# Performance work log

Hardware: AMD Instinct MI355X
Metric: run time of the kernel (lower is better)

## Reference

```python
import jax, jax.numpy as jnp
import numpy as np

NUM_HEADS = 16
LN_EPS = 1e-5


def _layer_norm(x, g, b):
    m = x.mean(-1, keepdims=True)
    v = x.var(-1, keepdims=True)
    return (x - m) / jnp.sqrt(v + LN_EPS) * g + b


def setup_inputs() -> dict:
    key = jax.random.key(0)
    ks = jax.random.split(key, 4)
    Bq, Bk, Nk, C = 128, 128, 256, 1024
    return {
        "qx": jax.random.normal(ks[0], (Bq, 1, C), jnp.float32),
        "kx": jax.random.normal(ks[1], (Bk, Nk, C), jnp.float32),
        "gq": jnp.ones((C,), jnp.float32),
        "bq": jnp.zeros((C,), jnp.float32),
        "gk": jnp.ones((C,), jnp.float32),
        "bk": jnp.zeros((C,), jnp.float32),
        "Wq": jax.random.normal(ks[2], (C, C), jnp.float32) * (C ** -0.5),
        "Wk": jax.random.normal(ks[3], (C, C), jnp.float32) * (C ** -0.5),
    }


def reference(qx, kx, gq, bq, gk, bk, Wq, Wk):
    H = NUM_HEADS
    Bq, _, C = qx.shape  # qx: [Bq, 1, C]
    Bk, Nk, _ = kx.shape  # kx: [Bk, Nk, C]
    hd = C // H
    scale = hd ** -0.5
    # LayerNorm + linear projections (nn.Linear: x @ W.T, no bias)
    q = (_layer_norm(qx, gq, bq) @ Wq.T).reshape(Bq, H, hd)       # [Bq, H, hd] (Nq=1 squeezed)
    k = (_layer_norm(kx, gk, bk) @ Wk.T).reshape(Bk, Nk, H, hd)   # [Bk, Nk, H, hd]
    # Full bipartite cross-batch attention scores: [Bq, Bk, H, Nk]
    attn = jnp.einsum('qhc,knhc->qkhn', q, k) * scale
    attn = jax.nn.softmax(attn, axis=-1)
    # v = kx broadcast over heads in original einsum 'khnc,qkhn->qkc';
    # equivalent: sum attn over heads, then contract over Nk.
    w = attn.sum(axis=2)                                           # [Bq, Bk, Nk]
    x = jnp.einsum('knc,qkn->qkc', kx, w)                          # [Bq, Bk, C]
    return x
```

## Files before the change

### kernel.cpp

```cpp
#include <hip/hip_runtime.h>


typedef unsigned short ushort_t;
typedef __bf16 bf16x8 __attribute__((ext_vector_type(8)));
typedef float f32x4 __attribute__((ext_vector_type(4)));

#define AS1 __attribute__((address_space(1)))
#define AS3 __attribute__((address_space(3)))

__device__ __forceinline__ void gload_lds16(const void* g, void* l) {
  __builtin_amdgcn_global_load_lds((const AS1 unsigned int*)g, (AS3 unsigned int*)l, 16, 0, 0);
}

__device__ __forceinline__ ushort_t f2bf(float f) {
  unsigned u = __float_as_uint(f);
  unsigned r = u + 0x7FFFu + ((u >> 16) & 1u);
  return (ushort_t)(r >> 16);
}

__global__ __launch_bounds__(256) void cvt_bf16_kernel(const float* __restrict__ src,
                                                       ushort_t* __restrict__ dst, int n4) {
  int i = blockIdx.x * 256 + threadIdx.x;
  if (i < n4) {
    float4 v = ((const float4*)src)[i];
    ushort4 o;
    o.x = f2bf(v.x); o.y = f2bf(v.y); o.z = f2bf(v.z); o.w = f2bf(v.w);
    ((ushort4*)dst)[i] = o;
  }
}

__global__ __launch_bounds__(256) void ln_kernel(const float* __restrict__ kx,
                                                 const float* __restrict__ qx,
                                                 const float* __restrict__ gk,
                                                 const float* __restrict__ bk,
                                                 const float* __restrict__ gq,
                                                 const float* __restrict__ bq,
                                                 ushort_t* __restrict__ kln,
                                                 ushort_t* __restrict__ qln) {
  int row = blockIdx.x;
  const float* src; ushort_t* dst; const float* g; const float* bb;
  if (row < 32768) {
    src = kx + (size_t)row * 1024; dst = kln + (size_t)row * 1024; g = gk; bb = bk;
  } else {
    int r = row - 32768;
    src = qx + (size_t)r * 1024; dst = qln + (size_t)r * 1024; g = gq; bb = bq;
  }
  int tid = threadIdx.x;
  float4 v = ((const float4*)src)[tid];
  float s  = v.x + v.y + v.z + v.w;
  float s2 = v.x*v.x + v.y*v.y + v.z*v.z + v.w*v.w;
  #pragma unroll
  for (int off = 1; off < 64; off <<= 1) {
    s  += __shfl_xor(s, off);
    s2 += __shfl_xor(s2, off);
  }
  __shared__ float red[8];
  int wid = tid >> 6, lane = tid & 63;
  if (lane == 0) { red[wid] = s; red[4 + wid] = s2; }
  __syncthreads();
  s  = red[0] + red[1] + red[2] + red[3];
  s2 = red[4] + red[5] + red[6] + red[7];
  float mean = s * (1.0f / 1024.0f);
  float var  = s2 * (1.0f / 1024.0f) - mean * mean;
  float rstd = rsqrtf(var + 1e-5f);
  float4 gg = ((const float4*)g)[tid];
  float4 b4 = ((const float4*)bb)[tid];
  ushort4 o;
  o.x = f2bf((v.x - mean) * rstd * gg.x + b4.x);
  o.y = f2bf((v.y - mean) * rstd * gg.y + b4.y);
  o.z = f2bf((v.z - mean) * rstd * gg.z + b4.z);
  o.w = f2bf((v.w - mean) * rstd * gg.w + b4.w);
  ((ushort4*)dst)[tid] = o;
}

#define BM 128
#define BN 128
#define BK 32

__global__ __launch_bounds__(256) void gemm_bt_kernel(const ushort_t* __restrict__ A,
                                                      const ushort_t* __restrict__ Bt,
                                                      ushort_t* __restrict__ C,
                                                      int M, int N, int K) {
  __shared__ ushort_t As[2][BM * BK];
  __shared__ ushort_t Bs[2][BN * BK];
  const int tid  = threadIdx.x;
  const int lane = tid & 63;
  const int wid  = tid >> 6;

  const int Mt = M >> 7, Nt = N >> 7;
  const int nwg = Mt * Nt;
  const int qq = nwg >> 3, r8 = nwg & 7;
  const int xcd = blockIdx.x & 7, idx = blockIdx.x >> 3;
  const int wg = (xcd < r8 ? xcd * (qq + 1) : r8 * (qq + 1) + (xcd - r8) * qq) + idx;
  const int mt = wg / Nt, nt = wg - mt * Nt;
  const size_t m0 = (size_t)mt * BM, n0 = (size_t)nt * BN;

  const int NTILE = K / BK;
  const int rlo = lane >> 2;
  const int cl  = lane & 3;

  f32x4 acc[4][4];
  #pragma unroll
  for (int i = 0; i < 4; ++i)
    #pragma unroll
    for (int j = 0; j < 4; ++j) acc[i][j] = (f32x4){0.f, 0.f, 0.f, 0.f};

  #pragma unroll
  for (int c = 0; c < 2; ++c) {
    int row = (wid << 5) + (c << 4) + rlo;
    int gch = cl ^ (row & 3);
    gload_lds16(A  + (m0 + row) * (size_t)K + gch * 8, &As[0][((wid << 5) + (c << 4)) * BK]);
    gload_lds16(Bt + (n0 + row) * (size_t)K + gch * 8, &Bs[0][((wid << 5) + (c << 4)) * BK]);
  }

  const int g = lane >> 4, rr = lane & 15;
  const int wr = wid >> 1, wc = wid & 1;

  for (int t = 0; t < NTILE; ++t) {
    __syncthreads();
    if (t + 1 < NTILE) {
      int k0 = (t + 1) * BK;
      #pragma unroll
      for (int c = 0; c < 2; ++c) {
        int row = (wid << 5) + (c << 4) + rlo;
        int gch = cl ^ (row & 3);
        gload_lds16(A  + (m0 + row) * (size_t)K + k0 + gch * 8,
                    &As[(t + 1) & 1][((wid << 5) + (c << 4)) * BK]);
        gload_lds16(Bt + (n0 + row) * (size_t)K + k0 + gch * 8,
                    &Bs[(t + 1) & 1][((wid << 5) + (c << 4)) * BK]);
      }
    }
    const ushort_t* as = As[t & 1];
    const ushort_t* bs = Bs[t & 1];
    bf16x8 af[4], bfr[4];
    #pragma unroll
    for (int i = 0; i < 4; ++i) {
      int rowA = (wr << 6) + (i << 4) + rr;
      int chA  = g ^ (rowA & 3);
      af[i] = *(const bf16x8*)&as[rowA * BK + chA * 8];
      int rowB = (wc << 6) + (i << 4) + rr;
      int chB  = g ^ (rowB & 3);
      bfr[i] = *(const bf16x8*)&bs[rowB * BK + chB * 8];
    }
    #pragma unroll
    for (int i = 0; i < 4; ++i)
      #pragma unroll
      for (int j = 0; j < 4; ++j)
        acc[i][j] = __builtin_amdgcn_mfma_f32_16x16x32_bf16(af[i], bfr[j], acc[i][j], 0, 0, 0);
  }

  #pragma unroll
  for (int i = 0; i < 4; ++i)
    #pragma unroll
    for (int j = 0; j < 4; ++j)
      #pragma unroll
      for (int rg = 0; rg < 4; ++rg) {
        size_t row = m0 + (wr << 6) + (i << 4) + (g << 2) + rg;
        size_t col = n0 + (wc << 6) + (j << 4) + rr;
        C[row * (size_t)N + col] = f2bf(acc[i][j][rg]);
      }
}

__global__ __launch_bounds__(256, 2) void attn_kernel(const ushort_t* __restrict__ qp,
                                                      const ushort_t* __restrict__ kk,
                                                      const float* __restrict__ kx,
                                                      float* __restrict__ xout) {
  __shared__ float pbuf[32][260];
  __shared__ ushort_t wlds[32 * 256];

  const int tid = threadIdx.x, lane = tid & 63, wid = tid >> 6;
  const int g = lane >> 4, rr = lane & 15;

  const int b = blockIdx.x;
  const int wg = (b & 7) * 64 + (b >> 3);
  const int kb = wg >> 2;
  const int q0 = (wg & 3) * 32;

  const int qg = wid & 1, hs = wid >> 1;
  const int q16 = q0 + (qg << 4);

  float w_acc[16][4];
  #pragma unroll
  for (int t = 0; t < 16; ++t)
    #pragma unroll
    for (int r = 0; r < 4; ++r) w_acc[t][r] = 0.f;

  const ushort_t* qrow = qp + (size_t)(q16 + rr) * 1024;
  const ushort_t* krow = kk + ((size_t)kb * 256 + rr) * 1024;

  for (int hp = 0; hp < 8; ++hp) {
    const int h = hp * 2 + hs;
    const int co = h * 64 + g * 8;
    bf16x8 aq0 = *(const bf16x8*)(qrow + co);
    bf16x8 aq1 = *(const bf16x8*)(qrow + co + 32);
    f32x4 s[16];
    #pragma unroll
    for (int t = 0; t < 16; ++t) {
      const ushort_t* kr = krow + (size_t)(t * 16) * 1024 + co;
      bf16x8 b0 = *(const bf16x8*)(kr);
      bf16x8 b1 = *(const bf16x8*)(kr + 32);
      f32x4 a = (f32x4){0.f, 0.f, 0.f, 0.f};
      a = __builtin_amdgcn_mfma_f32_16x16x32_bf16(aq0, b0, a, 0, 0, 0);
      a = __builtin_amdgcn_mfma_f32_16x16x32_bf16(aq1, b1, a, 0, 0, 0);
      s[t] = a;
    }
    #pragma unroll
    for (int r = 0; r < 4; ++r) {
      float mx = s[0][r];
      #pragma unroll
      for (int t = 1; t < 16; ++t) mx = fmaxf(mx, s[t][r]);
      mx = fmaxf(mx, __shfl_xor(mx, 1));
      mx = fmaxf(mx, __shfl_xor(mx, 2));
      mx = fmaxf(mx, __shfl_xor(mx, 4));
      mx = fmaxf(mx, __shfl_xor(mx, 8));
      float sum = 0.f;
      float e[16];
      #pragma unroll
      for (int t = 0; t < 16; ++t) {
        e[t] = __expf((s[t][r] - mx) * 0.125f);
        sum += e[t];
      }
      sum += __shfl_xor(sum, 1);
      sum += __shfl_xor(sum, 2);
      sum += __shfl_xor(sum, 4);
      sum += __shfl_xor(sum, 8);
      float inv = 1.0f / sum;
      #pragma unroll
      for (int t = 0; t < 16; ++t) w_acc[t][r] += e[t] * inv;
    }
  }

  __syncthreads();
  if (hs == 1) {
    #pragma unroll
    for (int t = 0; t < 16; ++t)
      #pragma unroll
      for (int r = 0; r < 4; ++r)
        pbuf[(qg << 4) + (g << 2) + r][t * 16 + rr] = w_acc[t][r];
  }
  __syncthreads();
  if (hs == 0) {
    #pragma unroll
    for (int t = 0; t < 16; ++t)
      #pragma unroll
      for (int r = 0; r < 4; ++r) {
        int q = (qg << 4) + (g << 2) + r;
        int n = t * 16 + rr;
        float v = w_acc[t][r] + pbuf[q][n];
        wlds[q * 256 + (((n >> 3) ^ (q & 7)) << 3) + (n & 7)] = f2bf(v);
      }
  }
  __syncthreads();

  const int cw = wid << 8;
  f32x4 acc2[2][16];
  #pragma unroll
  for (int m2 = 0; m2 < 2; ++m2)
    #pragma unroll
    for (int t2 = 0; t2 < 16; ++t2) acc2[m2][t2] = (f32x4){0.f, 0.f, 0.f, 0.f};

  for (int nc = 0; nc < 8; ++nc) {
    const int n0 = nc * 32;
    bf16x8 pa[2];
    #pragma unroll
    for (int m2 = 0; m2 < 2; ++m2) {
      int q = (m2 << 4) + rr;
      pa[m2] = *(const bf16x8*)&wlds[q * 256 + ((((nc << 2) + g) ^ (q & 7)) << 3)];
    }
    const float* kxb = kx + ((size_t)kb * 256 + n0 + g * 8) * 1024;
    #pragma unroll
    for (int t2 = 0; t2 < 16; ++t2) {
      const int c = cw + t2 * 16 + rr;
      float f[8];
      #pragma unroll
      for (int j = 0; j < 8; ++j) f[j] = kxb[(size_t)j * 1024 + c];
      bf16x8 bb;
      #pragma unroll
      for (int j = 0; j < 8; ++j) bb[j] = (__bf16)f[j];
      acc2[0][t2] = __builtin_amdgcn_mfma_f32_16x16x32_bf16(pa[0], bb, acc2[0][t2], 0, 0, 0);
      acc2[1][t2] = __builtin_amdgcn_mfma_f32_16x16x32_bf16(pa[1], bb, acc2[1][t2], 0, 0, 0);
    }
  }

  #pragma unroll
  for (int m2 = 0; m2 < 2; ++m2)
    #pragma unroll
    for (int t2 = 0; t2 < 16; ++t2)
      #pragma unroll
      for (int rg = 0; rg < 4; ++rg) {
        int q = q0 + (m2 << 4) + (g << 2) + rg;
        int c = cw + t2 * 16 + rr;
        xout[((size_t)q * 128 + kb) * 1024 + c] = acc2[m2][t2][rg];
      }
}

extern "C" void kernel_launch(void* const* d_in, const int* in_sizes, int n_in,
                              void* d_out, int out_size, void* d_ws, size_t ws_size,
                              hipStream_t stream) {
  const float* qx = (const float*)d_in[0];
  const float* kx = (const float*)d_in[1];
  const float* gq = (const float*)d_in[2];
  const float* bq = (const float*)d_in[3];
  const float* gk = (const float*)d_in[4];
  const float* bk = (const float*)d_in[5];
  const float* Wq = (const float*)d_in[6];
  const float* Wk = (const float*)d_in[7];

  char* ws = (char*)d_ws;
  ushort_t* kkp   = (ushort_t*)(ws);
  ushort_t* qln   = (ushort_t*)(ws + 67108864);
  ushort_t* qproj = (ushort_t*)(ws + 67371008);
  ushort_t* Wqb   = (ushort_t*)(ws + 67633152);
  ushort_t* Wkb   = (ushort_t*)(ws + 69730304);
  ushort_t* kln  = (ushort_t*)d_out;
  float*    xout = (float*)d_out;

  cvt_bf16_kernel<<<1024, 256, 0, stream>>>(Wq, Wqb, 262144);
  cvt_bf16_kernel<<<1024, 256, 0, stream>>>(Wk, Wkb, 262144);
  ln_kernel<<<32896, 256, 0, stream>>>(kx, qx, gk, bk, gq, bq, kln, qln);
  gemm_bt_kernel<<<8, 256, 0, stream>>>(qln, Wqb, qproj, 128, 1024, 1024);
  gemm_bt_kernel<<<2048, 256, 0, stream>>>(kln, Wkb, kkp, 32768, 1024, 1024);
  attn_kernel<<<512, 256, 0, stream>>>(qproj, kkp, kx, xout);
}
```

Measured before the change: 283.1 us.

## Split fused attention into separate scores and PV kernels with larger tiles

The fused attention kernel becomes two kernels. A scores kernel uses 512 threads, splits the 16 heads across four waves, reduces their partial softmax weights through LDS in two stages, and writes the bf16 head-summed weights to a workspace buffer. A separate PV kernel then computes the 128x128 output tiles per key batch as a GEMM. In that GEMM each block covers all 128 queries, so every kx element is read and converted once per block instead of four times. The cost is one extra launch and a global round trip for the weight matrix, and the workspace layout is rearranged so wbuf reuses the qln region.

```diff
diff --git a/kernel.cpp b/kernel.cpp
--- a/kernel.cpp
+++ b/kernel.cpp
@@ -161,12 +161,10 @@
       }
 }
 
-__global__ __launch_bounds__(256, 2) void attn_kernel(const ushort_t* __restrict__ qp,
-                                                      const ushort_t* __restrict__ kk,
-                                                      const float* __restrict__ kx,
-                                                      float* __restrict__ xout) {
-  __shared__ float pbuf[32][260];
-  __shared__ ushort_t wlds[32 * 256];
+__global__ __launch_bounds__(512, 4) void scores_kernel(const ushort_t* __restrict__ qp,
+                                                        const ushort_t* __restrict__ kk,
+                                                        ushort_t* __restrict__ wbuf) {
+  __shared__ float pbuf[2][2][16][258];
 
   const int tid = threadIdx.x, lane = tid & 63, wid = tid >> 6;
   const int g = lane >> 4, rr = lane & 15;
@@ -176,7 +174,7 @@
   const int kb = wg >> 2;
   const int q0 = (wg & 3) * 32;
 
-  const int qg = wid & 1, hs = wid >> 1;
+  const int qg = wid >> 2, hs = wid & 3;
   const int q16 = q0 + (qg << 4);
 
   float w_acc[16][4];
@@ -188,8 +186,8 @@
   const ushort_t* qrow = qp + (size_t)(q16 + rr) * 1024;
   const ushort_t* krow = kk + ((size_t)kb * 256 + rr) * 1024;
 
-  for (int hp = 0; hp < 8; ++hp) {
-    const int h = hp * 2 + hs;
+  for (int hp = 0; hp < 4; ++hp) {
+    const int h = hp * 4 + hs;
     const int co = h * 64 + g * 8;
     bf16x8 aq0 = *(const bf16x8*)(qrow + co);
     bf16x8 aq1 = *(const bf16x8*)(qrow + co + 32);
@@ -231,66 +229,96 @@
   }
 
   __syncthreads();
-  if (hs == 1) {
+  if (hs >= 2) {
     #pragma unroll
     for (int t = 0; t < 16; ++t)
       #pragma unroll
       for (int r = 0; r < 4; ++r)
-        pbuf[(qg << 4) + (g << 2) + r][t * 16 + rr] = w_acc[t][r];
+        pbuf[qg][hs - 2][(g << 2) + r][t * 16 + rr] = w_acc[t][r];
+  }
+  __syncthreads();
+  if (hs < 2) {
+    #pragma unroll
+    for (int t = 0; t < 16; ++t)
+      #pragma unroll
+      for (int r = 0; r < 4; ++r)
+        w_acc[t][r] += pbuf[qg][hs][(g << 2) + r][t * 16 + rr];
+    if (hs == 1) {
+      #pragma unroll
+      for (int t = 0; t < 16; ++t)
+        #pragma unroll
+        for (int r = 0; r < 4; ++r)
+          pbuf[qg][1][(g << 2) + r][t * 16 + rr] = w_acc[t][r];
+    }
   }
   __syncthreads();
   if (hs == 0) {
+    ushort_t* wb = wbuf + (size_t)kb * 32768;
     #pragma unroll
     for (int t = 0; t < 16; ++t)
       #pragma unroll
       for (int r = 0; r < 4; ++r) {
-        int q = (qg << 4) + (g << 2) + r;
-        int n = t * 16 + rr;
-        float v = w_acc[t][r] + pbuf[q][n];
-        wlds[q * 256 + (((n >> 3) ^ (q & 7)) << 3) + (n & 7)] = f2bf(v);
-      }
-  }
-  __syncthreads();
-
-  const int cw = wid << 8;
-  f32x4 acc2[2][16];
-  #pragma unroll
-  for (int m2 = 0; m2 < 2; ++m2)
-    #pragma unroll
-    for (int t2 = 0; t2 < 16; ++t2) acc2[m2][t2] = (f32x4){0.f, 0.f, 0.f, 0.f};
+        float v = w_acc[t][r] + pbuf[qg][1][(g << 2) + r][t * 16 + rr];
+        wb[(size_t)(q16 + (g << 2) + r) * 256 + t * 16 + rr] = f2bf(v);
+      }
+  }
+}
+
+__global__ __launch_bounds__(256, 4) void pv_kernel(const ushort_t* __restrict__ wbuf,
+                                                    const float* __restrict__ kx,
+                                                    float* __restrict__ xout) {
+  const int tid = threadIdx.x, lane = tid & 63, wid = tid >> 6;
+  const int g = lane >> 4, rr = lane & 15;
+
+  const int b = blockIdx.x;
+  const int wg = (b & 7) * 128 + (b >> 3);
+  const int kb = wg >> 3;
+  const int c0 = (wg & 7) * 128;
+
+  const int wr = wid >> 1, wc = wid & 1;
+
+  f32x4 acc[4][4];
+  #pragma unroll
+  for (int i = 0; i < 4; ++i)
+    #pragma unroll
+    for (int j = 0; j < 4; ++j) acc[i][j] = (f32x4){0.f, 0.f, 0.f, 0.f};
+
+  const ushort_t* wb = wbuf + (size_t)kb * 32768;
+  const float* kxb = kx + (size_t)kb * 256 * 1024;
 
   for (int nc = 0; nc < 8; ++nc) {
-    const int n0 = nc * 32;
-    bf16x8 pa[2];
-    #pragma unroll
-    for (int m2 = 0; m2 < 2; ++m2) {
-      int q = (m2 << 4) + rr;
-      pa[m2] = *(const bf16x8*)&wlds[q * 256 + ((((nc << 2) + g) ^ (q & 7)) << 3)];
-    }
-    const float* kxb = kx + ((size_t)kb * 256 + n0 + g * 8) * 1024;
-    #pragma unroll
-    for (int t2 = 0; t2 < 16; ++t2) {
-      const int c = cw + t2 * 16 + rr;
+    const int n0 = nc * 32 + g * 8;
+    bf16x8 af[4];
+    #pragma unroll
+    for (int i = 0; i < 4; ++i) {
+      int q = (wr << 6) + (i << 4) + rr;
+      af[i] = *(const bf16x8*)(wb + (size_t)q * 256 + n0);
+    }
+    #pragma unroll
+    for (int j = 0; j < 4; ++j) {
+      int c = c0 + (wc << 6) + (j << 4) + rr;
+      const float* src = kxb + (size_t)n0 * 1024 + c;
       float f[8];
       #pragma unroll
-      for (int j = 0; j < 8; ++j) f[j] = kxb[(size_t)j * 1024 + c];
+      for (int jj = 0; jj < 8; ++jj) f[jj] = src[(size_t)jj * 1024];
       bf16x8 bb;
       #pragma unroll
-      for (int j = 0; j < 8; ++j) bb[j] = (__bf16)f[j];
-      acc2[0][t2] = __builtin_amdgcn_mfma_f32_16x16x32_bf16(pa[0], bb, acc2[0][t2], 0, 0, 0);
-      acc2[1][t2] = __builtin_amdgcn_mfma_f32_16x16x32_bf16(pa[1], bb, acc2[1][t2], 0, 0, 0);
-    }
-  }
-
-  #pragma unroll
-  for (int m2 = 0; m2 < 2; ++m2)
-    #pragma unroll
-    for (int t2 = 0; t2 < 16; ++t2)
+      for (int jj = 0; jj < 8; ++jj) bb[jj] = (__bf16)f[jj];
+      #pragma unroll
+      for (int i = 0; i < 4; ++i)
+        acc[i][j] = __builtin_amdgcn_mfma_f32_16x16x32_bf16(af[i], bb, acc[i][j], 0, 0, 0);
+    }
+  }
+
+  #pragma unroll
+  for (int i = 0; i < 4; ++i)
+    #pragma unroll
+    for (int j = 0; j < 4; ++j)
       #pragma unroll
       for (int rg = 0; rg < 4; ++rg) {
-        int q = q0 + (m2 << 4) + (g << 2) + rg;
-        int c = cw + t2 * 16 + rr;
-        xout[((size_t)q * 128 + kb) * 1024 + c] = acc2[m2][t2][rg];
+        int q = (wr << 6) + (i << 4) + (g << 2) + rg;
+        int c = c0 + (wc << 6) + (j << 4) + rr;
+        xout[((size_t)q * 128 + kb) * 1024 + c] = acc[i][j][rg];
       }
 }
 
@@ -308,10 +336,11 @@
 
   char* ws = (char*)d_ws;
   ushort_t* kkp   = (ushort_t*)(ws);
-  ushort_t* qln   = (ushort_t*)(ws + 67108864);
-  ushort_t* qproj = (ushort_t*)(ws + 67371008);
-  ushort_t* Wqb   = (ushort_t*)(ws + 67633152);
-  ushort_t* Wkb   = (ushort_t*)(ws + 69730304);
+  ushort_t* qproj = (ushort_t*)(ws + 67108864);
+  ushort_t* wbuf  = (ushort_t*)(ws + 67371008);
+  ushort_t* qln   = (ushort_t*)(ws + 67371008);
+  ushort_t* Wqb   = (ushort_t*)(ws + 67371008 + 262144);
+  ushort_t* Wkb   = (ushort_t*)(ws + 67371008 + 2359296);
   ushort_t* kln  = (ushort_t*)d_out;
   float*    xout = (float*)d_out;
 
@@ -320,5 +349,6 @@
   ln_kernel<<<32896, 256, 0, stream>>>(kx, qx, gk, bk, gq, bq, kln, qln);
   gemm_bt_kernel<<<8, 256, 0, stream>>>(qln, Wqb, qproj, 128, 1024, 1024);
   gemm_bt_kernel<<<2048, 256, 0, stream>>>(kln, Wkb, kkp, 32768, 1024, 1024);
-  attn_kernel<<<512, 256, 0, stream>>>(qproj, kkp, kx, xout);
-}
+  scores_kernel<<<512, 512, 0, stream>>>(qproj, kkp, wbuf);
+  pv_kernel<<<1024, 256, 0, stream>>>(wbuf, kx, xout);
+}
```

Measured after the change: 337.2 us. 19.1% more time.
